# Performance work log

Hardware: AMD Instinct MI355X
Metric: run time of the kernel (lower is better)

## Reference

```python
import jax, jax.numpy as jnp
import numpy as np

BODY_EDGES = [(0, 2), (0, 5), (2, 7), (5, 8), (11, 12), (0, 11), (0, 12), (7, 11), (8, 12), (11, 13), (13, 15), (12, 14), (14, 16), (11, 23), (12, 24), (23, 24), (11, 24), (12, 23)]
N_JOINTS = 33
N_FEAT = 52
HIDDEN = 128
BN_EPS = 1e-5


def _make_adj():
    a = np.eye(N_JOINTS, dtype=np.float32)
    for i, j in BODY_EDGES:
        a[i, j] = 1.0
        a[j, i] = 1.0
    deg = np.clip(a.sum(1), 1.0, None)
    d = deg ** -0.5
    return jnp.asarray(d[:, None] * a * d[None, :])


def setup_inputs() -> dict:
    key = jax.random.key(0)
    ks = iter(jax.random.split(key, 40))
    B, T = 64, 256
    def lin(k, i, o):
        return jax.random.normal(k, (i, o), jnp.float32) / np.sqrt(i)
    inp = {
        'x': jax.random.normal(next(ks), (B, T, N_JOINTS, N_FEAT), jnp.float32),
        'adj': _make_adj(),
        # layer 0: in 52 -> out 128 (has skip linear)
        'W0': lin(next(ks), N_FEAT, HIDDEN), 'b0': jax.random.normal(next(ks), (HIDDEN,)) * 0.02,
        'S0': lin(next(ks), N_FEAT, HIDDEN), 'sb0': jax.random.normal(next(ks), (HIDDEN,)) * 0.02,
        'g0': 1.0 + 0.1 * jax.random.normal(next(ks), (HIDDEN,)), 'be0': 0.1 * jax.random.normal(next(ks), (HIDDEN,)),
        'm0': 0.1 * jax.random.normal(next(ks), (HIDDEN,)), 'v0': 1.0 + 0.1 * jax.random.uniform(next(ks), (HIDDEN,)),
        # layers 1,2: 128 -> 128 (identity skip)
        'W1': lin(next(ks), HIDDEN, HIDDEN), 'b1': jax.random.normal(next(ks), (HIDDEN,)) * 0.02,
        'g1': 1.0 + 0.1 * jax.random.normal(next(ks), (HIDDEN,)), 'be1': 0.1 * jax.random.normal(next(ks), (HIDDEN,)),
        'm1': 0.1 * jax.random.normal(next(ks), (HIDDEN,)), 'v1': 1.0 + 0.1 * jax.random.uniform(next(ks), (HIDDEN,)),
        'W2': lin(next(ks), HIDDEN, HIDDEN), 'b2': jax.random.normal(next(ks), (HIDDEN,)) * 0.02,
        'g2': 1.0 + 0.1 * jax.random.normal(next(ks), (HIDDEN,)), 'be2': 0.1 * jax.random.normal(next(ks), (HIDDEN,)),
        'm2': 0.1 * jax.random.normal(next(ks), (HIDDEN,)), 'v2': 1.0 + 0.1 * jax.random.uniform(next(ks), (HIDDEN,)),
        # temporal attention MLP: 128 -> 128 -> 1
        'tW1': lin(next(ks), HIDDEN, HIDDEN), 'tb1': jax.random.normal(next(ks), (HIDDEN,)) * 0.02,
        'tW2': lin(next(ks), HIDDEN, 1), 'tb2': jax.random.normal(next(ks), (1,)) * 0.02,
    }
    return inp


def _gcn(h, adj, W, b, g, be, m, v, skip):
    # adjacency mix: [B*T, J, D_in]
    a = jnp.einsum('nm,bmd->bnd', adj, h)
    z = a @ W + b
    z = (z - m) * jax.lax.rsqrt(v + BN_EPS) * g + be  # eval-mode BatchNorm1d
    return jax.nn.gelu(z, approximate=False) + skip


def reference(x, adj, W0, b0, S0, sb0, g0, be0, m0, v0,
              W1, b1, g1, be1, m1, v1,
              W2, b2, g2, be2, m2, v2,
              tW1, tb1, tW2, tb2):
    B, T, J, Fd = x.shape
    h = x.reshape(B * T, J, Fd)
    h = _gcn(h, adj, W0, b0, g0, be0, m0, v0, h @ S0 + sb0)
    h = _gcn(h, adj, W1, b1, g1, be1, m1, v1, h)
    h = _gcn(h, adj, W2, b2, g2, be2, m2, v2, h)
    # dropout inactive (eval mode)
    xt = h.mean(axis=1).reshape(B, T, -1)                  # [B, T, H]
    score = jax.nn.gelu(xt @ tW1 + tb1, approximate=False) @ tW2 + tb2  # [B, T, 1]
    attn = jax.nn.softmax(score, axis=1)
    return (xt * attn).sum(axis=1)                         # [B, H]
```

## Files before the change

kernel.cpp:

```cpp
#include <hip/hip_runtime.h>
#include <hip/hip_bf16.h>
#include <math.h>


#define NJ 33
#define NF 52
#define NH 128
#define NT 256
#define NB 64
#define NSAMP (NB*NT)
#define SPB 2
#define NBLKS (NSAMP/SPB)
#define HSTR 136
#define PSTR 40

typedef unsigned short u16;
typedef _Float16 f16;
typedef f16   half8 __attribute__((ext_vector_type(8)));
typedef f16   h2    __attribute__((ext_vector_type(2)));
typedef float f32x4 __attribute__((ext_vector_type(4)));

#define HO_W0    0
#define HO_S0    8192
#define HO_W1    16384
#define HO_W2    32768
#define HO_TW1   49152
#define HO_ADJ32 65536
#define H_TOTAL  66560
#define FO_BASE  (H_TOTAL/2)
#define FO_A0    (FO_BASE+0)
#define FO_SB0   (FO_BASE+768)
#define FO_TB1   (FO_BASE+896)
#define FO_TW2   (FO_BASE+1024)
#define FO_XT    (FO_BASE+1152)
#define FO_SC    (FO_XT + NSAMP*NH)

__device__ __forceinline__ float bf2f(u16 u) { return __uint_as_float(((unsigned)u) << 16); }
__device__ __forceinline__ float ldv(const void* p, long i, int f) {
    float r;
    if (f) r = bf2f(((const u16*)p)[i]);
    else   r = ((const float*)p)[i];
    return r;
}
__device__ int detect_bf16(const void* p) {
    const u16* q = (const u16*)p;
    int nz = 0, ok = 0;
#pragma unroll
    for (int k = 0; k < 64; k++) {
        u16 u = q[k];
        if (u & 0x7FFF) {
            nz++;
            int e = (u >> 7) & 0xFF;
            ok += (e >= 0x40 && e <= 0xBF) ? 1 : 0;
        }
    }
    return (nz == 0) || (ok * 20 >= nz * 19);
}

__device__ __forceinline__ float gelu_t(float x) {
    float xc = fminf(fmaxf(x, -8.f), 8.f);
    float u  = xc * fmaf(xc * xc, 0.10294324f, 2.3022082f);
#if __has_builtin(__builtin_amdgcn_exp2f)
    float e  = __builtin_amdgcn_exp2f(u);
#else
    float e  = exp2f(u);
#endif
#if __has_builtin(__builtin_amdgcn_rcpf)
    float tt = (e - 1.f) * __builtin_amdgcn_rcpf(e + 1.f);
#else
    float tt = (e - 1.f) / (e + 1.f);
#endif
    float hx = 0.5f * x;
    return fmaf(hx, tt, hx);
}

#define MFMA16(a, b, c) __builtin_amdgcn_mfma_f32_16x16x32_f16(a, b, c, 0, 0, 0)

__global__ __launch_bounds__(256) void prep(
    const void* adj,
    const void* W0, const void* b0, const void* S0, const void* sb0,
    const void* g0, const void* be0, const void* m0, const void* v0,
    const void* W1, const void* b1, const void* g1, const void* be1, const void* m1, const void* v1,
    const void* W2, const void* b2, const void* g2, const void* be2, const void* m2, const void* v2,
    const void* tW1, const void* tb1, const void* tW2,
    void* ws)
{
    f16* H = (f16*)ws; float* F = (float*)ws;
    const int bi = blockIdx.x, t = threadIdx.x;
    if (bi == 0) {
        const int fW = detect_bf16(W0), fS = detect_bf16(S0);
        for (int i = t; i < NF * 128; i += 256) {
            int k = i >> 7, n = i & 127;
            H[HO_W0 + n * 64 + k] = (f16)ldv(W0, i, fW);
            H[HO_S0 + n * 64 + k] = (f16)ldv(S0, i, fS);
        }
        for (int i = t; i < 128 * 16; i += 256) {
            int n = i >> 4, k = 48 + (i & 15);
            if (k >= NF) { H[HO_W0 + n * 64 + k] = (f16)0.f; H[HO_S0 + n * 64 + k] = (f16)0.f; }
        }
    } else if (bi == 1) {
        const int f = detect_bf16(W1);
        for (int i = t; i < 128 * 128; i += 256) {
            int k = i >> 7, n = i & 127;
            H[HO_W1 + n * 128 + k] = (f16)ldv(W1, i, f);
        }
    } else if (bi == 2) {
        const int f = detect_bf16(W2);
        for (int i = t; i < 128 * 128; i += 256) {
            int k = i >> 7, n = i & 127;
            H[HO_W2 + n * 128 + k] = (f16)ldv(W2, i, f);
        }
    } else if (bi == 3) {
        const int f = detect_bf16(tW1);
        for (int i = t; i < 128 * 128; i += 256) {
            int k = i >> 7, n = i & 127;
            H[HO_TW1 + n * 128 + k] = (f16)ldv(tW1, i, f);
        }
    } else {
        if (t < 128) {
            int c = t;
            {
                float g = ldv(g0,c,detect_bf16(g0)), be = ldv(be0,c,detect_bf16(be0));
                float m = ldv(m0,c,detect_bf16(m0)), v = ldv(v0,c,detect_bf16(v0));
                float b = ldv(b0,c,detect_bf16(b0));
                float A = g * rsqrtf(v + 1e-5f);
                F[FO_A0 + 0*256 + c] = A; F[FO_A0 + 0*256 + 128 + c] = (b - m)*A + be;
            }
            {
                float g = ldv(g1,c,detect_bf16(g1)), be = ldv(be1,c,detect_bf16(be1));
                float m = ldv(m1,c,detect_bf16(m1)), v = ldv(v1,c,detect_bf16(v1));
                float b = ldv(b1,c,detect_bf16(b1));
                float A = g * rsqrtf(v + 1e-5f);
                F[FO_A0 + 1*256 + c] = A; F[FO_A0 + 1*256 + 128 + c] = (b - m)*A + be;
            }
            {
                float g = ldv(g2,c,detect_bf16(g2)), be = ldv(be2,c,detect_bf16(be2));
                float m = ldv(m2,c,detect_bf16(m2)), v = ldv(v2,c,detect_bf16(v2));
                float b = ldv(b2,c,detect_bf16(b2));
                float A = g * rsqrtf(v + 1e-5f);
                F[FO_A0 + 2*256 + c] = A; F[FO_A0 + 2*256 + 128 + c] = (b - m)*A + be;
            }
            F[FO_SB0 + c] = ldv(sb0, c, detect_bf16(sb0));
            F[FO_TB1 + c] = ldv(tb1, c, detect_bf16(tb1));
            F[FO_TW2 + c] = ldv(tW2, c, detect_bf16(tW2));
        }
        const int fA = detect_bf16(adj);
        for (int i = t; i < 1024; i += 256) {
            int r = i >> 5, c = i & 31;
            float v = (r < 25 && c < 25) ? ldv(adj, (long)r*NJ + c, fA) : 0.f;
            H[HO_ADJ32 + i] = (f16)v;
        }
    }
}

#define PTWRITE(ACC)                                                            \
    _Pragma("unroll")                                                           \
    for (int mt = 0; mt < 4; mt++) {                                            \
        const int fF = mt >> 1;                                                 \
        const int jb = (mt & 1) * 16;                                           \
        _Pragma("unroll")                                                       \
        for (int nt = 0; nt < 2; nt++) {                                        \
            f16* pp = Pt + (fF*128 + (nt ? c1 : c0))*PSTR;                      \
            _Pragma("unroll")                                                   \
            for (int r2 = 0; r2 < 4; r2 += 2) {                                 \
                int j0 = jb + q*4 + r2;                                         \
                if (j0 + 1 < 25) {                                              \
                    h2 v2w = { (f16)ACC[mt][nt][r2], (f16)ACC[mt][nt][r2+1] };  \
                    *(h2*)(pp + j0) = v2w;                                      \
                } else if (j0 < 25) {                                           \
                    pp[j0] = (f16)ACC[mt][nt][r2];                              \
                }                                                               \
            }                                                                   \
        }                                                                       \
    }

#define ADJEPI(L, WRHB) {                                                       \
    f32x4 zac[2][2][2];                                                         \
    _Pragma("unroll")                                                           \
    for (int fF = 0; fF < 2; fF++) {                                            \
        _Pragma("unroll")                                                       \
        for (int nt = 0; nt < 2; nt++) {                                        \
            half8 bz = *(const half8*)(Pt + (fF*128 + (nt?c1:c0))*PSTR + q*8);  \
            zac[fF][0][nt] = MFMA16(afadj0, bz, z4);                            \
            zac[fF][1][nt] = MFMA16(afadj1, bz, z4);                            \
        }                                                                       \
    }                                                                           \
    _Pragma("unroll")                                                           \
    for (int nt = 0; nt < 2; nt++) {                                            \
        const int cc = nt ? c1 : c0;                                            \
        const float Av = rA[L][nt], Dv = rD[L][nt];                             \
        _Pragma("unroll")                                                       \
        for (int fF = 0; fF < 2; fF++) {                                        \
            _Pragma("unroll")                                                   \
            for (int m2 = 0; m2 < 2; m2++) {                                    \
                _Pragma("unroll")                                               \
                for (int r4 = 0; r4 < 4; r4++) {                                \
                    float zv = (m2 == 0) ? zac[fF][0][nt][r4]                   \
                             : (jlt[r4] ? zac[fF][1][nt][r4]                    \
                                        : acc[2*fF+1][nt][r4]);                 \
                    float hnew = gelu_t(fmaf(zv, Av, Dv)) + hz[fF][m2][nt][r4]; \
                    hz[fF][m2][nt][r4] = hnew;                                  \
                    if (WRHB)                                                   \
                        hb[((2*fF+m2)*16 + q*4 + r4)*HSTR + cc] = (f16)hnew;    \
                }                                                               \
            }                                                                   \
            {                                                                   \
                float hnew = gelu_t(fmaf(acc[4][nt][fF], Av, Dv)) + h32[fF][nt];\
                h32[fF][nt] = (q == 0) ? hnew : 0.f;                            \
                if (WRHB && q == 0)                                             \
                    hb[(64 + fF)*HSTR + cc] = (f16)hnew;                        \
            }                                                                   \
        }                                                                       \
    }                                                                           \
}

#define GEMM128(WOFF)                                                           \
    {                                                                           \
        half8 bf[2][4];                                                         \
        _Pragma("unroll")                                                       \
        for (int nt = 0; nt < 2; nt++)                                          \
            _Pragma("unroll")                                                   \
            for (int ks = 0; ks < 4; ks++)                                      \
                bf[nt][ks] = *(const half8*)(HW + (WOFF) + (nt?c1:c0)*128 + ks*32 + q*8); \
        _Pragma("unroll")                                                       \
        for (int mt = 0; mt < 5; mt++) { acc[mt][0] = z4; acc[mt][1] = z4; }    \
        _Pragma("unroll")                                                       \
        for (int mt = 0; mt < 5; mt++) {                                        \
            const int m = mt*16 + ml;                                           \
            _Pragma("unroll")                                                   \
            for (int ks = 0; ks < 4; ks++) {                                    \
                half8 af = *(const half8*)(hb + m*HSTR + ks*32 + q*8);          \
                acc[mt][0] = MFMA16(af, bf[0][ks], acc[mt][0]);                 \
                acc[mt][1] = MFMA16(af, bf[1][ks], acc[mt][1]);                 \
            }                                                                   \
        }                                                                       \
    }

__global__ __launch_bounds__(256) void gcn_mfma(const void* __restrict__ x,
                                                void* __restrict__ ws)
{
    const f16* HW = (const f16*)ws;
    float* F = (float*)ws;
    float* xt_g = F + FO_XT;
    float* sc_g = F + FO_SC;

    __shared__ __align__(16) f16 hb[80 * HSTR];
    __shared__ __align__(16) f16 Pt[2 * 128 * PSTR];
    __shared__ float rbuf4[4];
    __shared__ int sfx;
    float* xtb = (float*)Pt;

    const int t = threadIdx.x, lane = t & 63, wv = t >> 6;
    const int q = lane >> 4, ml = lane & 15;
    const int n0 = wv * 32;
    const int c0 = n0 + ml, c1 = n0 + 16 + ml;
    const f32x4 z4 = {0.f, 0.f, 0.f, 0.f};
    const bool jlt[4] = { q <= 2, q <= 1, q <= 1, q <= 1 };
    const half8 zero8 = {(f16)0.f,(f16)0.f,(f16)0.f,(f16)0.f,(f16)0.f,(f16)0.f,(f16)0.f,(f16)0.f};

    if (t == 0) sfx = detect_bf16(x);
#pragma unroll
    for (int i = t; i < 512; i += 256) {
        int fF = i >> 8, rem = i & 255, n = rem >> 1, ch = rem & 1;
        *(half8*)(Pt + (fF*128 + n)*PSTR + 24 + ch*8) = zero8;
    }

    float rA[3][2], rD[3][2];
#pragma unroll
    for (int L = 0; L < 3; L++) {
        rA[L][0] = F[FO_A0 + L*256 + c0];        rA[L][1] = F[FO_A0 + L*256 + c1];
        rD[L][0] = F[FO_A0 + L*256 + 128 + c0];  rD[L][1] = F[FO_A0 + L*256 + 128 + c1];
    }
    const float sb0a = F[FO_SB0 + c0], sb0b = F[FO_SB0 + c1];
    half8 afadj0 = *(const half8*)(HW + HO_ADJ32 + ml*32 + q*8);
    half8 afadj1 = *(const half8*)(HW + HO_ADJ32 + (16+ml)*32 + q*8);
    __syncthreads();

    {
        const int fX = sfx;
        const long xb = (long)blockIdx.x * (SPB * NJ * NF);
#pragma unroll 1
        for (int it = 0; it < 3; it++) {
            int g = t + it * 256;
            if (g < 66 * 8) {
                int r = g >> 3, blk = g & 7;
                int fF = (r >= 33) ? 1 : 0;
                int j = r - 33 * fF;
                int fr = (j < 32) ? (fF * 32 + j) : (64 + fF);
                half8 o;
                if (!fX) {
                    const float* base = (const float*)x + xb + (long)r * NF + blk * 8;
                    if (blk < 6) {
                        float4 v0 = *(const float4*)base;
                        float4 v1 = *(const float4*)(base + 4);
                        o[0]=(f16)v0.x; o[1]=(f16)v0.y; o[2]=(f16)v0.z; o[3]=(f16)v0.w;
                        o[4]=(f16)v1.x; o[5]=(f16)v1.y; o[6]=(f16)v1.z; o[7]=(f16)v1.w;
                    } else if (blk == 6) {
                        float4 v0 = *(const float4*)base;
                        o = zero8;
                        o[0]=(f16)v0.x; o[1]=(f16)v0.y; o[2]=(f16)v0.z; o[3]=(f16)v0.w;
                    } else o = zero8;
                } else {
                    long rb = xb + (long)r * NF;
#pragma unroll
                    for (int i = 0; i < 8; i++) {
                        int cx = blk * 8 + i;
                        o[i] = (f16)(cx < NF ? bf2f(((const u16*)x)[rb + cx]) : 0.f);
                    }
                }
                *(half8*)(hb + fr * HSTR + blk * 8) = o;
            }
        }
    }
    __syncthreads();

    f32x4 acc[5][2];
    float hz[2][2][2][4];
    float h32[2][2];

    {
        half8 bw[2][2], bs[2][2];
#pragma unroll
        for (int nt = 0; nt < 2; nt++) {
            int n = nt ? c1 : c0;
#pragma unroll
            for (int ks = 0; ks < 2; ks++) {
                bw[nt][ks] = *(const half8*)(HW + HO_W0 + n*64 + ks*32 + q*8);
                bs[nt][ks] = *(const half8*)(HW + HO_S0 + n*64 + ks*32 + q*8);
            }
        }
        f32x4 acs[5][2];
#pragma unroll
        for (int mt = 0; mt < 5; mt++) { acc[mt][0]=z4; acc[mt][1]=z4; acs[mt][0]=z4; acs[mt][1]=z4; }
#pragma unroll
        for (int mt = 0; mt < 5; mt++) {
            const int m = mt*16 + ml;
            half8 a0 = *(const half8*)(hb + m*HSTR + q*8);
            half8 a1 = *(const half8*)(hb + m*HSTR + 32 + q*8);
            acc[mt][0] = MFMA16(a0, bw[0][0], acc[mt][0]);
            acc[mt][0] = MFMA16(a1, bw[0][1], acc[mt][0]);
            acc[mt][1] = MFMA16(a0, bw[1][0], acc[mt][1]);
            acc[mt][1] = MFMA16(a1, bw[1][1], acc[mt][1]);
            acs[mt][0] = MFMA16(a0, bs[0][0], acs[mt][0]);
            acs[mt][0] = MFMA16(a1, bs[0][1], acs[mt][0]);
            acs[mt][1] = MFMA16(a0, bs[1][0], acs[mt][1]);
            acs[mt][1] = MFMA16(a1, bs[1][1], acs[mt][1]);
        }
        __syncthreads();
        PTWRITE(acc)
#pragma unroll
        for (int fF = 0; fF < 2; fF++)
#pragma unroll
            for (int m2 = 0; m2 < 2; m2++)
#pragma unroll
                for (int nt = 0; nt < 2; nt++)
#pragma unroll
                    for (int r4 = 0; r4 < 4; r4++)
                        hz[fF][m2][nt][r4] = acs[2*fF+m2][nt][r4] + (nt ? sb0b : sb0a);
#pragma unroll
        for (int fF = 0; fF < 2; fF++)
#pragma unroll
            for (int nt = 0; nt < 2; nt++)
                h32[fF][nt] = (q == 0) ? (acs[4][nt][fF] + (nt ? sb0b : sb0a)) : 0.f;
        ADJEPI(0, 1)
        __syncthreads();
    }

    GEMM128(HO_W1)
    __syncthreads();
    PTWRITE(acc)
    ADJEPI(1, 1)
    __syncthreads();

    GEMM128(HO_W2)
    __syncthreads();
    PTWRITE(acc)
    ADJEPI(2, 0)
    __syncthreads();

#pragma unroll
    for (int fF = 0; fF < 2; fF++)
#pragma unroll
        for (int nt = 0; nt < 2; nt++) {
            float s = h32[fF][nt];
#pragma unroll
            for (int m2 = 0; m2 < 2; m2++)
#pragma unroll
                for (int r4 = 0; r4 < 4; r4++) s += hz[fF][m2][nt][r4];
            s += __shfl_xor(s, 16, 64);
            s += __shfl_xor(s, 32, 64);
            float xtc = s * (1.0f / 33.0f);
            if (q == 0) {
                int cc = nt ? c1 : c0;
                xtb[fF * 128 + cc] = xtc;
                xt_g[((long)blockIdx.x * SPB + fF) * NH + cc] = xtc;
            }
        }
    __syncthreads();

    {
        const int fF = t >> 7, c = t & 127;
        float u = 0.f;
#pragma unroll
        for (int kk = 0; kk < 16; kk++) {
            half8 wv8 = *(const half8*)(HW + HO_TW1 + c*128 + kk*8);
#pragma unroll
            for (int i = 0; i < 8; i++)
                u = fmaf(xtb[fF*128 + kk*8 + i], (float)wv8[i], u);
        }
        float r = gelu_t(u + F[FO_TB1 + c]) * F[FO_TW2 + c];
#pragma unroll
        for (int off = 32; off > 0; off >>= 1) r += __shfl_xor(r, off, 64);
        if (lane == 0) rbuf4[wv] = r;
        __syncthreads();
        if (t == 0) {
            sc_g[blockIdx.x * SPB + 0] = rbuf4[0] + rbuf4[1];
            sc_g[blockIdx.x * SPB + 1] = rbuf4[2] + rbuf4[3];
        }
    }
}

__global__ __launch_bounds__(256) void attn_pool(
    const void* __restrict__ x,
    const float* __restrict__ xt_ws, const float* __restrict__ score_ws,
    void* __restrict__ out)
{
    __shared__ float ew[NT];
    __shared__ float red[8];
    __shared__ float pb[256];
    __shared__ int sfx2;
    const int t = threadIdx.x, lane = t & 63, wv = t >> 6;
    const int b = blockIdx.x >> 2, qr = blockIdx.x & 3;

    if (t == 0) sfx2 = detect_bf16(x);
    float sv = score_ws[b * NT + t];
    float m = sv;
#pragma unroll
    for (int off = 32; off > 0; off >>= 1) m = fmaxf(m, __shfl_xor(m, off, 64));
    if (lane == 0) red[wv] = m;
    __syncthreads();
    float mx = fmaxf(fmaxf(red[0], red[1]), fmaxf(red[2], red[3]));
    float e = __expf(sv - mx);
    ew[t] = e;
    float d = e;
#pragma unroll
    for (int off = 32; off > 0; off >>= 1) d += __shfl_xor(d, off, 64);
    if (lane == 0) red[4 + wv] = d;
    __syncthreads();
    float den = red[4] + red[5] + red[6] + red[7];

    const int cl = t & 31, ch = t >> 5;
    const int c = qr * 32 + cl;
    float a = 0.f;
#pragma unroll 4
    for (int i = ch * 32; i < ch * 32 + 32; i++)
        a = fmaf(ew[i], xt_ws[((long)b * NT + i) * NH + c], a);
    pb[t] = a;
    __syncthreads();
    if (t < 128) pb[t] += pb[t + 128];
    __syncthreads();
    if (t < 64) pb[t] += pb[t + 64];
    __syncthreads();
    if (t < 32) {
        float r = (pb[t] + pb[t + 32]) / den;
        if (sfx2) ((__hip_bfloat16*)out)[b * NH + qr * 32 + t] = __float2bfloat16(r);
        else      ((float*)out)[b * NH + qr * 32 + t] = r;
    }
}

extern "C" void kernel_launch(void* const* d_in, const int* in_sizes, int n_in,
                              void* d_out, int out_size, void* d_ws, size_t ws_size,
                              hipStream_t stream) {
    prep<<<5, 256, 0, stream>>>(
        d_in[1],
        d_in[2], d_in[3], d_in[4], d_in[5],
        d_in[6], d_in[7], d_in[8], d_in[9],
        d_in[10], d_in[11], d_in[12], d_in[13], d_in[14], d_in[15],
        d_in[16], d_in[17], d_in[18], d_in[19], d_in[20], d_in[21],
        d_in[22], d_in[23], d_in[24],
        d_ws);
    gcn_mfma<<<NBLKS, 256, 0, stream>>>(d_in[0], d_ws);
    float* F = (float*)d_ws;
    attn_pool<<<NB * 4, 256, 0, stream>>>(d_in[0], F + FO_XT, F + FO_SC, d_out);
}
```

Measured before the change: 576.9 us.

## Re-layout adjacency scratch into 8-wide chunks, simplify GELU, add occupancy hint

The per-block P scratch changes from a padded row-major layout (stride 40) to a chunked layout where each group of 8 joints for all 128 channels is contiguous. This is meant to reduce LDS bank conflicts on the half8 B-operand reads, and the scratch also gets smaller. The tanh-based GELU is rewritten as x - x/(e+1) with the input clamp removed, which saves a few ALU ops but can overflow exp2 for large |x| (the result degrades gracefully toward x or 0). The launch bounds also request 4 waves per SIMD, which may constrain register allocation.

```diff
diff --git a/kernel.cpp b/kernel.cpp
--- a/kernel.cpp
+++ b/kernel.cpp
@@ -12,7 +12,6 @@
 #define SPB 2
 #define NBLKS (NSAMP/SPB)
 #define HSTR 136
-#define PSTR 40
 
 typedef unsigned short u16;
 typedef _Float16 f16;
@@ -35,6 +34,8 @@
 #define FO_XT    (FO_BASE+1152)
 #define FO_SC    (FO_XT + NSAMP*NH)
 
+#define PT2(fF,qd,n) ((((fF)*4+(qd))*128+(n))*8)
+
 __device__ __forceinline__ float bf2f(u16 u) { return __uint_as_float(((unsigned)u) << 16); }
 __device__ __forceinline__ float ldv(const void* p, long i, int f) {
     float r;
@@ -58,20 +59,17 @@
 }
 
 __device__ __forceinline__ float gelu_t(float x) {
-    float xc = fminf(fmaxf(x, -8.f), 8.f);
-    float u  = xc * fmaf(xc * xc, 0.10294324f, 2.3022082f);
+    float u = x * fmaf(x * x, 0.10294324f, 2.3022082f);
 #if __has_builtin(__builtin_amdgcn_exp2f)
-    float e  = __builtin_amdgcn_exp2f(u);
+    float e = __builtin_amdgcn_exp2f(u);
 #else
-    float e  = exp2f(u);
+    float e = exp2f(u);
 #endif
 #if __has_builtin(__builtin_amdgcn_rcpf)
-    float tt = (e - 1.f) * __builtin_amdgcn_rcpf(e + 1.f);
+    return x - x * __builtin_amdgcn_rcpf(e + 1.f);
 #else
-    float tt = (e - 1.f) / (e + 1.f);
+    return x - x / (e + 1.f);
 #endif
-    float hx = 0.5f * x;
-    return fmaf(hx, tt, hx);
 }
 
 #define MFMA16(a, b, c) __builtin_amdgcn_mfma_f32_16x16x32_f16(a, b, c, 0, 0, 0)
@@ -160,15 +158,16 @@
         const int jb = (mt & 1) * 16;                                           \
         _Pragma("unroll")                                                       \
         for (int nt = 0; nt < 2; nt++) {                                        \
-            f16* pp = Pt + (fF*128 + (nt ? c1 : c0))*PSTR;                      \
+            const int cc = nt ? c1 : c0;                                        \
             _Pragma("unroll")                                                   \
             for (int r2 = 0; r2 < 4; r2 += 2) {                                 \
                 int j0 = jb + q*4 + r2;                                         \
+                f16* pp = Pt + PT2(fF, j0 >> 3, cc) + (j0 & 7);                 \
                 if (j0 + 1 < 25) {                                              \
                     h2 v2w = { (f16)ACC[mt][nt][r2], (f16)ACC[mt][nt][r2+1] };  \
-                    *(h2*)(pp + j0) = v2w;                                      \
+                    *(h2*)pp = v2w;                                             \
                 } else if (j0 < 25) {                                           \
-                    pp[j0] = (f16)ACC[mt][nt][r2];                              \
+                    *pp = (f16)ACC[mt][nt][r2];                                 \
                 }                                                               \
             }                                                                   \
         }                                                                       \
@@ -180,7 +179,7 @@
     for (int fF = 0; fF < 2; fF++) {                                            \
         _Pragma("unroll")                                                       \
         for (int nt = 0; nt < 2; nt++) {                                        \
-            half8 bz = *(const half8*)(Pt + (fF*128 + (nt?c1:c0))*PSTR + q*8);  \
+            half8 bz = *(const half8*)(Pt + PT2(fF, q, (nt?c1:c0)));            \
             zac[fF][0][nt] = MFMA16(afadj0, bz, z4);                            \
             zac[fF][1][nt] = MFMA16(afadj1, bz, z4);                            \
         }                                                                       \
@@ -236,8 +235,8 @@
         }                                                                       \
     }
 
-__global__ __launch_bounds__(256) void gcn_mfma(const void* __restrict__ x,
-                                                void* __restrict__ ws)
+__global__ __launch_bounds__(256, 4) void gcn_mfma(const void* __restrict__ x,
+                                                   void* __restrict__ ws)
 {
     const f16* HW = (const f16*)ws;
     float* F = (float*)ws;
@@ -245,7 +244,7 @@
     float* sc_g = F + FO_SC;
 
     __shared__ __align__(16) f16 hb[80 * HSTR];
-    __shared__ __align__(16) f16 Pt[2 * 128 * PSTR];
+    __shared__ __align__(16) f16 Pt[2 * 4 * 128 * 8];
     __shared__ float rbuf4[4];
     __shared__ int sfx;
     float* xtb = (float*)Pt;
@@ -259,10 +258,9 @@
     const half8 zero8 = {(f16)0.f,(f16)0.f,(f16)0.f,(f16)0.f,(f16)0.f,(f16)0.f,(f16)0.f,(f16)0.f};
 
     if (t == 0) sfx = detect_bf16(x);
-#pragma unroll
-    for (int i = t; i < 512; i += 256) {
-        int fF = i >> 8, rem = i & 255, n = rem >> 1, ch = rem & 1;
-        *(half8*)(Pt + (fF*128 + n)*PSTR + 24 + ch*8) = zero8;
+    {
+        int fF = t >> 7, n = t & 127;
+        *(half8*)(Pt + PT2(fF, 3, n)) = zero8;
     }
 
     float rA[3][2], rD[3][2];
```

Result: slower. 652.5 us (+13.1%).
